# Performance work log

Hardware: AMD Instinct MI355X
Metric: run time of the kernel (lower is better)

## Reference

```python
import jax, jax.numpy as jnp
import numpy as np

N = 65536      # nodes
D = 1024       # d_model
H = 16         # nhead
HD = D // H    # head_dim = 64
K = 4096       # neighbors with local bias
D_EXTRA = 20   # local_bias feature dim
BIAS_DIM = 40  # rbf(16)+seqsep(4)+extra(20)
RES = 0.5      # res_scale
EPS = 1e-5


def _ln(x, w, b):
    mu = x.mean(-1, keepdims=True)
    var = ((x - mu) ** 2).mean(-1, keepdims=True)
    return (x - mu) * jax.lax.rsqrt(var + EPS) * w + b


def setup_inputs() -> dict:
    key = jax.random.key(0)
    ks = jax.random.split(key, 12)
    s = 0.02
    f32 = jnp.float32
    return {
        "h": jax.random.normal(ks[0], (N, D), f32),
        "rbf_ic": jax.random.uniform(ks[1], (N, 16), f32),
        "seqsep_ic": jax.random.uniform(ks[2], (N, 4), f32),
        "local_bias": jax.random.normal(ks[3], (K, D_EXTRA), f32),
        "norm_c_w": jnp.ones((D,), f32), "norm_c_b": jnp.zeros((D,), f32),
        "norm_all_w": jnp.ones((D,), f32), "norm_all_b": jnp.zeros((D,), f32),
        "Wq": jax.random.normal(ks[4], (D, D), f32) * s,
        "Wk": jax.random.normal(ks[5], (D, D), f32) * s,
        "Wv": jax.random.normal(ks[6], (D, D), f32) * s,
        "Wo": jax.random.normal(ks[7], (D, D), f32) * s,
        "Wbias": jax.random.normal(ks[8], (H, BIAS_DIM), f32) * s,
        "gate_W": jax.random.normal(ks[9], (D, 2 * D), f32) * s,
        "gate_b": jnp.zeros((D,), f32),
        "fuse_W1": jax.random.normal(ks[10], (D, 2 * D), f32) * s,
        "fuse_b1": jnp.zeros((D,), f32),
        "fuse_W2": jax.random.normal(ks[11], (D, D), f32) * s,
        "fuse_b2": jnp.zeros((D,), f32),
        "nbr_idx": jnp.arange(K, dtype=jnp.int32),
        "center_idx": 1000,
    }


def _forward(h, rbf_ic, seqsep_ic, local_bias,
             norm_c_w, norm_c_b, norm_all_w, norm_all_b,
             Wq, Wk, Wv, Wo, Wbias,
             gate_W, gate_b, fuse_W1, fuse_b1, fuse_W2, fuse_b2,
             nbr_idx, center_idx):
    c = center_idx
    # bias features: rbf || seqsep || scatter(local_bias)  -> (N, BIAS_DIM)
    full_bias = jnp.zeros((N, D_EXTRA), h.dtype).at[nbr_idx].set(local_bias)
    bias_feat = jnp.concatenate([rbf_ic, seqsep_ic, full_bias], axis=-1)

    h_c = _ln(h[c:c + 1], norm_c_w, norm_c_b)      # (1, D)
    h_all = _ln(h, norm_all_w, norm_all_b)          # (N, D)

    q = (h_c @ Wq.T).reshape(H, HD)                 # (H, HD)
    k = (h_all @ Wk.T).reshape(N, H, HD)            # (N, H, HD)
    v = (h_all @ Wv.T).reshape(N, H, HD)

    logits = jnp.einsum('hd,nhd->hn', q, k) / np.sqrt(HD)   # (H, N)
    logits = logits + (bias_feat @ Wbias.T).T                # add geo bias per head
    w = jax.nn.softmax(logits, axis=-1)                      # (H, N)

    out_center = jnp.einsum('hn,nhd->hd', w, v).reshape(1, D)
    delta_c = out_center @ Wo.T
    h_c_new = h[c:c + 1] + RES * delta_c            # (1, D)

    g = jnp.broadcast_to(h_c_new, (N, D))
    h_cat = jnp.concatenate([h, g], axis=-1)        # (N, 2D)
    gate = jax.nn.sigmoid(h_cat @ gate_W.T + gate_b)
    fused = jax.nn.silu(h_cat @ fuse_W1.T + fuse_b1) @ fuse_W2.T + fuse_b2
    h_new = h + RES * (gate * fused)
    h_new = h_new.at[c].set(h_c_new[0])
    return h_new


def reference(h, rbf_ic, seqsep_ic, local_bias,
              norm_c_w, norm_c_b, norm_all_w, norm_all_b,
              Wq, Wk, Wv, Wo, Wbias,
              gate_W, gate_b, fuse_W1, fuse_b1, fuse_W2, fuse_b2,
              nbr_idx, center_idx):
    return _forward(h, rbf_ic, seqsep_ic, local_bias,
                    norm_c_w, norm_c_b, norm_all_w, norm_all_b,
                    Wq, Wk, Wv, Wo, Wbias,
                    gate_W, gate_b, fuse_W1, fuse_b1, fuse_W2, fuse_b2,
                    nbr_idx, center_idx)
```

## Files before the change

### kernel.cpp

```cpp
#include <hip/hip_runtime.h>
#include <hip/hip_bf16.h>

#define NN 65536
#define DM 1024
#define NH 16
#define KNB 4096
#define DEX 20
#define EPSV 1e-5f

typedef __attribute__((ext_vector_type(8))) short bf16x8;
typedef __attribute__((ext_vector_type(4))) float f32x4;

__device__ __forceinline__ unsigned short f2bf(float f){
  unsigned u = __builtin_bit_cast(unsigned, f);
  u += 0x7fffu + ((u >> 16) & 1u);
  return (unsigned short)(u >> 16);
}
__device__ __forceinline__ float bf2f(unsigned short s){
  return __builtin_bit_cast(float, ((unsigned)s) << 16);
}
__device__ __forceinline__ float wred(float v){
  #pragma unroll
  for (int s = 32; s; s >>= 1) v += __shfl_down(v, s);
  return v;
}

__device__ __forceinline__ bf16x8 ldsr128(const unsigned short* p){
  bf16x8 r;
  unsigned a = (unsigned)(size_t)(const __attribute__((address_space(3))) void*)p;
  asm volatile("ds_read_b128 %0, %1" : "=v"(r) : "v"(a));
  return r;
}

__global__ void k_scatter(const float* __restrict__ lb, const int* __restrict__ nidx,
                          float* __restrict__ extra){
  int i = blockIdx.x * 256 + threadIdx.x;
  if (i < KNB * DEX){
    int j = i / DEX, col = i - j * DEX;
    extra[(size_t)nidx[j] * DEX + col] = lb[i];
  }
}

__global__ void k_convw(const float* __restrict__ gateW, const float* __restrict__ fuseW1,
                        const float* __restrict__ fuseW2,
                        unsigned short* __restrict__ Wcomb, unsigned short* __restrict__ W2b){
  int i = blockIdx.x * 256 + threadIdx.x;
  if (i < 2048 * 1024){
    int o = i >> 10, d = i & 1023;
    float v = (o < 1024) ? gateW[(size_t)o * 2048 + d] : fuseW1[(size_t)(o - 1024) * 2048 + d];
    Wcomb[i] = f2bf(v);
  } else {
    int j = i - 2048 * 1024;
    W2b[j] = f2bf(fuseW2[j]);
  }
}

__global__ void k_cln(const float* __restrict__ h, const int* __restrict__ cidx,
                      const float* __restrict__ cw, const float* __restrict__ cb,
                      float* __restrict__ hcln){
  int t = threadIdx.x, lane = t & 63, wid = t >> 6;
  int c = *cidx;
  const float4 x = *(const float4*)(h + (size_t)c * DM + t * 4);
  float s  = x.x + x.y + x.z + x.w;
  float ss = x.x * x.x + x.y * x.y + x.z * x.z + x.w * x.w;
  __shared__ float rs[4], rq[4];
  s = wred(s); ss = wred(ss);
  if (lane == 0){ rs[wid] = s; rq[wid] = ss; }
  __syncthreads();
  float mean = (rs[0] + rs[1] + rs[2] + rs[3]) * (1.0f / DM);
  float var  = (rq[0] + rq[1] + rq[2] + rq[3]) * (1.0f / DM) - mean * mean;
  float rstd = rsqrtf(var + EPSV);
  const float4 w = *(const float4*)(cw + t * 4);
  const float4 b = *(const float4*)(cb + t * 4);
  float4 o;
  o.x = (x.x - mean) * rstd * w.x + b.x;
  o.y = (x.y - mean) * rstd * w.y + b.y;
  o.z = (x.z - mean) * rstd * w.z + b.z;
  o.w = (x.w - mean) * rstd * w.w + b.w;
  *(float4*)(hcln + t * 4) = o;
}

__global__ void k_q(const float* __restrict__ hcln, const float* __restrict__ Wq,
                    float* __restrict__ q){
  int lane = threadIdx.x & 63, wid = threadIdx.x >> 6;
  float hv[16];
  #pragma unroll
  for (int j = 0; j < 16; j++) hv[j] = hcln[lane + 64 * j];
  #pragma unroll
  for (int oi = 0; oi < 4; oi++){
    int o = blockIdx.x * 16 + wid * 4 + oi;
    const float* wr = Wq + (size_t)o * DM;
    float a = 0.f;
    #pragma unroll
    for (int j = 0; j < 16; j++) a = fmaf(hv[j], wr[lane + 64 * j], a);
    a = wred(a);
    if (lane == 0) q[o] = a;
  }
}

__global__ void k_qkt(const float* __restrict__ q, const float* __restrict__ Wk,
                      float* __restrict__ qkt){
  int idx = blockIdx.x * 256 + threadIdx.x;
  int hh = idx >> 10, i = idx & 1023;
  float a = 0.f;
  #pragma unroll 8
  for (int d = 0; d < 64; d++) a = fmaf(q[hh * 64 + d], Wk[(size_t)(hh * 64 + d) * DM + i], a);
  qkt[idx] = a * 0.125f;
}

__global__ void k_c12(const float* __restrict__ qkt, const float* __restrict__ aw,
                      const float* __restrict__ ab, float* __restrict__ c12){
  const int hh = blockIdx.x >> 1, which = blockIdx.x & 1, lane = threadIdx.x;
  const float* src = which ? ab : aw;
  float a = 0.f;
  #pragma unroll
  for (int j = 0; j < 16; j++) a = fmaf(src[lane + 64 * j], qkt[hh * DM + lane + 64 * j], a);
  a = wred(a);
  if (lane == 0) c12[which * NH + hh] = a;
}

__global__ void k_qa(const float* __restrict__ qkt, const float* __restrict__ aw,
                     unsigned short* __restrict__ Qa){
  const int i = blockIdx.x * 256 + threadIdx.x;
  Qa[i] = f2bf(qkt[i] * aw[i & (DM - 1)]);
}

__global__ void k_bias(const float* __restrict__ rbf, const float* __restrict__ seqsep,
                       const float* __restrict__ extra, const float* __restrict__ wbias,
                       float* __restrict__ biasT){
  const int i = blockIdx.x * 256 + threadIdx.x;
  const int n = i >> 4, hh = i & 15;
  const float* wb = wbias + hh * 40;
  float bb = 0.f;
  #pragma unroll
  for (int j = 0; j < 16; j++) bb = fmaf(rbf[(size_t)n * 16 + j], wb[j], bb);
  #pragma unroll
  for (int j = 0; j < 4; j++)  bb = fmaf(seqsep[(size_t)n * 4 + j], wb[16 + j], bb);
  #pragma unroll
  for (int j = 0; j < 20; j++) bb = fmaf(extra[(size_t)n * DEX + j], wb[20 + j], bb);
  biasT[i] = bb;
}

__global__ void k_lnpass(const float* __restrict__ h, float* __restrict__ meanb,
                         float* __restrict__ rstdb, unsigned short* __restrict__ hbf){
  const int lane = threadIdx.x & 63, w = threadIdx.x >> 6;
  const int gw = blockIdx.x * 4 + w;
  #pragma unroll
  for (int rr = 0; rr < 2; rr++){
    const int n = gw * 2 + rr;
    const float* hp = h + (size_t)n * DM + lane * 16;
    const float4 x0 = *(const float4*)(hp);
    const float4 x1 = *(const float4*)(hp + 4);
    const float4 x2 = *(const float4*)(hp + 8);
    const float4 x3 = *(const float4*)(hp + 12);
    float s  = (x0.x + x0.y + x0.z + x0.w) + (x1.x + x1.y + x1.z + x1.w)
             + (x2.x + x2.y + x2.z + x2.w) + (x3.x + x3.y + x3.z + x3.w);
    float ss = x0.x*x0.x + x0.y*x0.y + x0.z*x0.z + x0.w*x0.w
             + x1.x*x1.x + x1.y*x1.y + x1.z*x1.z + x1.w*x1.w
             + x2.x*x2.x + x2.y*x2.y + x2.z*x2.z + x2.w*x2.w
             + x3.x*x3.x + x3.y*x3.y + x3.z*x3.z + x3.w*x3.w;
    #pragma unroll
    for (int m = 1; m < 64; m <<= 1){ s += __shfl_xor(s, m); ss += __shfl_xor(ss, m); }
    unsigned short* op = hbf + (size_t)n * DM + lane * 16;
    ushort4 o;
    o.x = f2bf(x0.x); o.y = f2bf(x0.y); o.z = f2bf(x0.z); o.w = f2bf(x0.w);
    *(ushort4*)(op) = o;
    o.x = f2bf(x1.x); o.y = f2bf(x1.y); o.z = f2bf(x1.z); o.w = f2bf(x1.w);
    *(ushort4*)(op + 4) = o;
    o.x = f2bf(x2.x); o.y = f2bf(x2.y); o.z = f2bf(x2.z); o.w = f2bf(x2.w);
    *(ushort4*)(op + 8) = o;
    o.x = f2bf(x3.x); o.y = f2bf(x3.y); o.z = f2bf(x3.z); o.w = f2bf(x3.w);
    *(ushort4*)(op + 12) = o;
    if (lane == 0){
      const float mean = s * (1.0f / DM);
      meanb[n] = mean;
      rstdb[n] = rsqrtf(ss * (1.0f / DM) - mean * mean + EPSV);
    }
  }
}

#define MFMA16(a, b, c) __builtin_amdgcn_mfma_f32_16x16x32_bf16(a, b, c, 0, 0, 0)

__launch_bounds__(256)
__global__ void k_logits(const unsigned short* __restrict__ hbf, const unsigned short* __restrict__ Qa,
                         const float* __restrict__ meanb, const float* __restrict__ rstdb,
                         const float* __restrict__ c12, const float* __restrict__ biasT,
                         float* __restrict__ logitsT){
  const int lane = threadIdx.x & 63, w = threadIdx.x >> 6;
  const int n0 = (blockIdx.x * 4 + w) * 16;
  const int fr = lane & 15, kq = lane >> 4;
  f32x4 acc = {0.f, 0.f, 0.f, 0.f};
  const unsigned short* ap = hbf + (size_t)(n0 + fr) * DM + kq * 8;
  const unsigned short* bp = Qa + fr * DM + kq * 8;
  #pragma unroll 4
  for (int kt = 0; kt < DM; kt += 64){
    const bf16x8 a0 = *(const bf16x8*)(ap + kt);
    const bf16x8 b0 = *(const bf16x8*)(bp + kt);
    const bf16x8 a1 = *(const bf16x8*)(ap + kt + 32);
    const bf16x8 b1 = *(const bf16x8*)(bp + kt + 32);
    acc = MFMA16(a0, b0, acc);
    acc = MFMA16(a1, b1, acc);
  }
  const float C1 = c12[fr], C2 = c12[NH + fr];
  #pragma unroll
  for (int r = 0; r < 4; r++){
    const int n = n0 + kq * 4 + r;
    const float mean = meanb[n], rstd = rstdb[n];
    logitsT[(size_t)n * NH + fr] = rstd * acc[r] - rstd * mean * C1 + C2
                                   + biasT[(size_t)n * NH + fr];
  }
}

__global__ void k_smpart(const float* __restrict__ logitsT, float* __restrict__ msp){
  const int t = threadIdx.x, lane = t & 63, w = t >> 6;
  const int hh = lane & 15, no = lane >> 4;
  const float* base = logitsT + ((size_t)blockIdx.x * 256 + w * 64) * NH;
  float m = -3.0e38f;
  #pragma unroll
  for (int it = 0; it < 16; it++)
    m = fmaxf(m, base[(it * 4 + no) * NH + hh]);
  m = fmaxf(m, __shfl_xor(m, 16));
  m = fmaxf(m, __shfl_xor(m, 32));
  float s = 0.f;
  #pragma unroll
  for (int it = 0; it < 16; it++)
    s += __expf(base[(it * 4 + no) * NH + hh] - m);
  s += __shfl_xor(s, 16);
  s += __shfl_xor(s, 32);
  __shared__ float sm[4][16], ssm[4][16];
  if (lane < 16){ sm[w][hh] = m; ssm[w][hh] = s; }
  __syncthreads();
  if (t < NH){
    const float M = fmaxf(fmaxf(sm[0][t], sm[1][t]), fmaxf(sm[2][t], sm[3][t]));
    const float S = ssm[0][t] * __expf(sm[0][t] - M) + ssm[1][t] * __expf(sm[1][t] - M)
                  + ssm[2][t] * __expf(sm[2][t] - M) + ssm[3][t] * __expf(sm[3][t] - M);
    msp[((size_t)blockIdx.x * NH + t) * 2]     = M;
    msp[((size_t)blockIdx.x * NH + t) * 2 + 1] = S;
  }
}

__global__ void k_smcomb(const float* __restrict__ msp, float* __restrict__ ms){
  const int lane = threadIdx.x;
  const int hh = lane & 15, g = lane >> 4;
  float M = -3.0e38f;
  for (int i = g; i < 256; i += 4) M = fmaxf(M, msp[((size_t)i * NH + hh) * 2]);
  M = fmaxf(M, __shfl_xor(M, 16));
  M = fmaxf(M, __shfl_xor(M, 32));
  float S = 0.f;
  for (int i = g; i < 256; i += 4)
    S += msp[((size_t)i * NH + hh) * 2 + 1] * __expf(msp[((size_t)i * NH + hh) * 2] - M);
  S += __shfl_xor(S, 16);
  S += __shfl_xor(S, 32);
  if (lane < NH){ ms[hh] = M; ms[16 + hh] = S; }
}

__global__ void k_expw(const float* __restrict__ logitsT, const float* __restrict__ ms,
                       float* __restrict__ wexp){
  const int i = blockIdx.x * 256 + threadIdx.x;
  const float4 v = ((const float4*)logitsT)[i];
  const int hb = (i & 3) * 4;
  float4 o;
  o.x = __expf(v.x - ms[hb]);
  o.y = __expf(v.y - ms[hb + 1]);
  o.z = __expf(v.z - ms[hb + 2]);
  o.w = __expf(v.w - ms[hb + 3]);
  ((float4*)wexp)[i] = o;
}

#define UB 256
__global__ void k_upart(const unsigned short* __restrict__ hbf, const float* __restrict__ meanb,
                        const float* __restrict__ rstdb, const float* __restrict__ aw,
                        const float* __restrict__ ab, const float* __restrict__ wexp,
                        float* __restrict__ upart){
  const int t = threadIdx.x, bb = blockIdx.x;
  const float4 w  = *(const float4*)(aw + t * 4);
  const float4 bv = *(const float4*)(ab + t * 4);
  float acc[NH][4];
  #pragma unroll
  for (int hh = 0; hh < NH; hh++){ acc[hh][0] = 0.f; acc[hh][1] = 0.f; acc[hh][2] = 0.f; acc[hh][3] = 0.f; }
  #pragma unroll 2
  for (int r = 0; r < NN / UB; r++){
    const int n = bb * (NN / UB) + r;
    const float mean = meanb[n], rstd = rstdb[n];
    const ushort4 hb = *(const ushort4*)(hbf + (size_t)n * DM + t * 4);
    const float l0 = (bf2f(hb.x) - mean) * rstd * w.x + bv.x;
    const float l1 = (bf2f(hb.y) - mean) * rstd * w.y + bv.y;
    const float l2 = (bf2f(hb.z) - mean) * rstd * w.z + bv.z;
    const float l3 = (bf2f(hb.w) - mean) * rstd * w.w + bv.w;
    const float4 e0 = *(const float4*)(wexp + (size_t)n * NH);
    const float4 e1 = *(const float4*)(wexp + (size_t)n * NH + 4);
    const float4 e2 = *(const float4*)(wexp + (size_t)n * NH + 8);
    const float4 e3 = *(const float4*)(wexp + (size_t)n * NH + 12);
#define ACC1(h, e) { acc[h][0] = fmaf(e, l0, acc[h][0]); acc[h][1] = fmaf(e, l1, acc[h][1]); \
                     acc[h][2] = fmaf(e, l2, acc[h][2]); acc[h][3] = fmaf(e, l3, acc[h][3]); }
    ACC1(0, e0.x)  ACC1(1, e0.y)  ACC1(2, e0.z)  ACC1(3, e0.w)
    ACC1(4, e1.x)  ACC1(5, e1.y)  ACC1(6, e1.z)  ACC1(7, e1.w)
    ACC1(8, e2.x)  ACC1(9, e2.y)  ACC1(10, e2.z) ACC1(11, e2.w)
    ACC1(12, e3.x) ACC1(13, e3.y) ACC1(14, e3.z) ACC1(15, e3.w)
#undef ACC1
  }
  #pragma unroll
  for (int hh = 0; hh < NH; hh++){
    float4 o; o.x = acc[hh][0]; o.y = acc[hh][1]; o.z = acc[hh][2]; o.w = acc[hh][3];
    *(float4*)(upart + ((size_t)bb * NH + hh) * DM + t * 4) = o;
  }
}

__global__ void k_ured1(const float* __restrict__ upart, float* __restrict__ up2){
  const int idx = (blockIdx.x & 63) * 256 + threadIdx.x;
  const int sl  = blockIdx.x >> 6;
  float s = 0.f;
  for (int b = sl * 16; b < sl * 16 + 16; b++) s += upart[(size_t)b * (NH * DM) + idx];
  up2[(size_t)sl * (NH * DM) + idx] = s;
}

__global__ void k_ured2(const float* __restrict__ up2, const float* __restrict__ ms,
                        float* __restrict__ u){
  const int idx = blockIdx.x * 256 + threadIdx.x;
  const int hh = idx >> 10;
  float s = 0.f;
  #pragma unroll
  for (int sl = 0; sl < 16; sl++) s += up2[(size_t)sl * (NH * DM) + idx];
  u[idx] = s / ms[16 + hh];
}

__global__ void k_oc(const float* __restrict__ u, const float* __restrict__ Wv,
                     float* __restrict__ oc){
  int lane = threadIdx.x & 63, wid = threadIdx.x >> 6;
  #pragma unroll
  for (int oi = 0; oi < 4; oi++){
    int o = blockIdx.x * 16 + wid * 4 + oi;
    const float* ur = u + (size_t)(o >> 6) * DM;
    const float* wr = Wv + (size_t)o * DM;
    float a = 0.f;
    #pragma unroll
    for (int j = 0; j < 16; j++) a = fmaf(ur[lane + 64 * j], wr[lane + 64 * j], a);
    a = wred(a);
    if (lane == 0) oc[o] = a;
  }
}

__global__ void k_delta(const float* __restrict__ oc, const float* __restrict__ Wo,
                        const float* __restrict__ h, const int* __restrict__ cidx,
                        float* __restrict__ hcnew){
  int lane = threadIdx.x & 63, wid = threadIdx.x >> 6;
  int c = *cidx;
  float ov[16];
  #pragma unroll
  for (int j = 0; j < 16; j++) ov[j] = oc[lane + 64 * j];
  #pragma unroll
  for (int oi = 0; oi < 4; oi++){
    int o = blockIdx.x * 16 + wid * 4 + oi;
    const float* wr = Wo + (size_t)o * DM;
    float a = 0.f;
    #pragma unroll
    for (int j = 0; j < 16; j++) a = fmaf(ov[j], wr[lane + 64 * j], a);
    a = wred(a);
    if (lane == 0) hcnew[o] = h[(size_t)c * DM + o] + 0.5f * a;
  }
}

__global__ void k_gbfb(const float* __restrict__ hcnew, const float* __restrict__ gateW,
                       const float* __restrict__ gateB, const float* __restrict__ fuseW1,
                       const float* __restrict__ fuseB1, float* __restrict__ gbtot,
                       float* __restrict__ fbtot){
  int lane = threadIdx.x & 63, wid = threadIdx.x >> 6;
  float hv[16];
  #pragma unroll
  for (int j = 0; j < 16; j++) hv[j] = hcnew[lane + 64 * j];
  #pragma unroll
  for (int oi = 0; oi < 4; oi++){
    int o = blockIdx.x * 16 + wid * 4 + oi;
    const float* gr = gateW + (size_t)o * 2048 + 1024;
    const float* fr = fuseW1 + (size_t)o * 2048 + 1024;
    float ga = 0.f, fa = 0.f;
    #pragma unroll
    for (int j = 0; j < 16; j++){
      ga = fmaf(hv[j], gr[lane + 64 * j], ga);
      fa = fmaf(hv[j], fr[lane + 64 * j], fa);
    }
    ga = wred(ga); fa = wred(fa);
    if (lane == 0){ gbtot[o] = ga + gateB[o]; fbtot[o] = fa + fuseB1[o]; }
  }
}

#define BM 256
#define BK 64
#define H128 ((size_t)128 * DM)
#define GLL16(gp, lp) __builtin_amdgcn_global_load_lds((const __attribute__((address_space(1))) void*)(gp), (__attribute__((address_space(3))) void*)(lp), 16, 0, 0)
#define SBAR() do { __builtin_amdgcn_sched_barrier(0); \
                    asm volatile("s_barrier" ::: "memory"); \
                    __builtin_amdgcn_sched_barrier(0); } while (0)

#define PHASE(BUF, Q, STG, STL, STK, DOVM) do {                                        \
    if ((Q) == 0){                                                                     \
      _Pragma("unroll")                                                                \
      for (int nj = 0; nj < 4; nj++){                                                  \
        bq[nj][0] = ldsr128(lB + (BUF)*16384 + bBase + nj*1024 + kOff0);               \
        bq[nj][1] = ldsr128(lB + (BUF)*16384 + bBase + nj*1024 + kOff1);               \
      }                                                                                \
    }                                                                                  \
    bf16x8 a00 = ldsr128(lA + (BUF)*16384 + aBase + (2*(Q))*1024   + kOff0);           \
    bf16x8 a01 = ldsr128(lA + (BUF)*16384 + aBase + (2*(Q))*1024   + kOff1);           \
    bf16x8 a10 = ldsr128(lA + (BUF)*16384 + aBase + (2*(Q)+1)*1024 + kOff0);           \
    bf16x8 a11 = ldsr128(lA + (BUF)*16384 + aBase + (2*(Q)+1)*1024 + kOff1);           \
    stage(STG, STL, STK);                                                              \
    SBAR();                                                                            \
    asm volatile("s_waitcnt lgkmcnt(0)" ::: "memory");                                 \
    __builtin_amdgcn_sched_barrier(0);                                                 \
    __builtin_amdgcn_s_setprio(1);                                                     \
    _Pragma("unroll")                                                                  \
    for (int nj = 0; nj < 4; nj++){                                                    \
      acc[2*(Q)][nj]   = MFMA16(a00, bq[nj][0], acc[2*(Q)][nj]);                       \
      acc[2*(Q)][nj]   = MFMA16(a01, bq[nj][1], acc[2*(Q)][nj]);                       \
      acc[2*(Q)+1][nj] = MFMA16(a10, bq[nj][0], acc[2*(Q)+1][nj]);                     \
      acc[2*(Q)+1][nj] = MFMA16(a11, bq[nj][1], acc[2*(Q)+1][nj]);                     \
    }                                                                                  \
    __builtin_amdgcn_s_setprio(0);                                                     \
    if (DOVM){ asm volatile("s_waitcnt vmcnt(4)" ::: "memory"); }                      \
    SBAR();                                                                            \
  } while (0)

template<int MODE>
__launch_bounds__(512, 2)
__global__ void k_gemm(const unsigned short* __restrict__ A, const unsigned short* __restrict__ B,
                       const float* __restrict__ bias0, const float* __restrict__ bias1,
                       const unsigned short* __restrict__ hsrcb, const unsigned short* __restrict__ gate,
                       unsigned short* __restrict__ og, unsigned short* __restrict__ ot,
                       float* __restrict__ of){
  __shared__ __attribute__((aligned(16))) unsigned short lA[32768];
  __shared__ __attribute__((aligned(16))) unsigned short lB[32768];
  const int NWG = (MODE == 0) ? 2048 : 1024;
  const int NYT = (MODE == 0) ? 8 : 4;
  const int bid = blockIdx.x;
  const int remap = (bid & 7) * (NWG >> 3) + (bid >> 3);
  const int m0 = (remap / NYT) * BM, n0 = (remap % NYT) * BM;

  const int tid = threadIdx.x, lane = tid & 63, w = tid >> 6;
  const int wm = w >> 2, wn = w & 3;

  f32x4 acc[8][4];
  #pragma unroll
  for (int i = 0; i < 8; i++){
    #pragma unroll
    for (int j = 0; j < 4; j++){ acc[i][j][0] = 0.f; acc[i][j][1] = 0.f; acc[i][j][2] = 0.f; acc[i][j][3] = 0.f; }
  }

  const int ln3 = lane >> 3;
  const size_t stRow0 = (size_t)(w * 16 + ln3);
  const int sxor = ((lane & 7) ^ ln3) * 8;
  const size_t srcOff0 = stRow0 * DM + sxor;
  const size_t srcOff1 = (stRow0 + 8) * DM + sxor;
  const int dst0 = w * 1024 + lane * 8;
  const int dst1 = dst0 + 512;

  const unsigned short* gA = A + (size_t)m0 * DM;
  const unsigned short* gB = B + (size_t)n0 * DM;

  auto stage = [&](const unsigned short* g, unsigned short* ldsr, int kt){
    GLL16(g + srcOff0 + kt * 64, ldsr + dst0);
    GLL16(g + srcOff1 + kt * 64, ldsr + dst1);
  };

  const int fr = lane & 15;
  const int kq = lane >> 4;
  const int kOff0 = ((kq)     ^ (lane & 7)) * 8;
  const int kOff1 = ((4 + kq) ^ (lane & 7)) * 8;
  const int aBase = wm * 8192 + fr * 64;
  const int bBase = (wn >> 1) * 8192 + ((wn & 1) * 64 + fr) * 64;

  bf16x8 bq[4][2];

  stage(gA,        lA,                0);
  stage(gA + H128, lA + 8192,         0);
  stage(gB,        lB,                0);
  stage(gB + H128, lB + 8192,         0);
  stage(gB,        lB + 16384,        1);
  stage(gB + H128, lB + 16384 + 8192, 1);
  asm volatile("s_waitcnt vmcnt(4)" ::: "memory");
  SBAR();

  #pragma unroll 1
  for (int i = 0; i < 8; i++){
    const int k0 = 2 * i;
    PHASE(0, 0, gA,        lA + 16384,        k0 + 1,        false);
    PHASE(0, 1, gA + H128, lA + 16384 + 8192, k0 + 1,        false);
    PHASE(0, 2, gB,        lB,                (k0 + 2) & 15, false);
    PHASE(0, 3, gB + H128, lB + 8192,         (k0 + 2) & 15, true);
    PHASE(1, 0, gA,        lA,                (k0 + 2) & 15, false);
    PHASE(1, 1, gA + H128, lA + 8192,         (k0 + 2) & 15, false);
    PHASE(1, 2, gB,        lB + 16384,        (k0 + 3) & 15, false);
    PHASE(1, 3, gB + H128, lB + 16384 + 8192, (k0 + 3) & 15, true);
  }

  const int r0 = kq * 4;
  #pragma unroll
  for (int mi = 0; mi < 8; mi++){
    #pragma unroll
    for (int nj = 0; nj < 4; nj++){
      const int gmb = m0 + wm * 128 + mi * 16 + r0;
      const int gn  = n0 + wn * 64 + nj * 16 + fr;
      #pragma unroll
      for (int r = 0; r < 4; r++){
        const int gm = gmb + r;
        const float x = acc[mi][nj][r];
        if (MODE == 0){
          if (gn < 1024){
            const float v = x + bias0[gn];
            og[(size_t)gm * DM + gn] = f2bf(1.0f / (1.0f + __expf(-v)));
          } else {
            const float v = x + bias1[gn - 1024];
            ot[(size_t)gm * DM + (gn - 1024)] = f2bf(v / (1.0f + __expf(-v)));
          }
        } else {
          const float v = x + bias0[gn];
          const float g = bf2f(gate[(size_t)gm * DM + gn]);
          of[(size_t)gm * DM + gn] = bf2f(hsrcb[(size_t)gm * DM + gn]) + 0.5f * g * v;
        }
      }
    }
  }
}

__global__ void k_fixc(const float* __restrict__ hcnew, const int* __restrict__ cidx,
                       float* __restrict__ out){
  int t = threadIdx.x;
  int c = *cidx;
  out[(size_t)c * DM + t] = hcnew[t];
}

extern "C" void kernel_launch(void* const* d_in, const int* in_sizes, int n_in,
                              void* d_out, int out_size, void* d_ws, size_t ws_size,
                              hipStream_t stream){
  const float* h      = (const float*)d_in[0];
  const float* rbf    = (const float*)d_in[1];
  const float* seqsep = (const float*)d_in[2];
  const float* localb = (const float*)d_in[3];
  const float* ncw    = (const float*)d_in[4];
  const float* ncb    = (const float*)d_in[5];
  const float* naw    = (const float*)d_in[6];
  const float* nab    = (const float*)d_in[7];
  const float* Wq     = (const float*)d_in[8];
  const float* Wk     = (const float*)d_in[9];
  const float* Wv     = (const float*)d_in[10];
  const float* Wo     = (const float*)d_in[11];
  const float* Wbias  = (const float*)d_in[12];
  const float* gateW  = (const float*)d_in[13];
  const float* gateB  = (const float*)d_in[14];
  const float* fuseW1 = (const float*)d_in[15];
  const float* fuseB1 = (const float*)d_in[16];
  const float* fuseW2 = (const float*)d_in[17];
  const float* fuseB2 = (const float*)d_in[18];
  const int*   nbr    = (const int*)d_in[19];
  const int*   cidx   = (const int*)d_in[20];
  float* out = (float*)d_out;

  char* p = (char*)d_ws;
  auto alloc = [&](size_t nb){ char* r = p; p += (nb + 255) & ~(size_t)255; return r; };
  float* extra   = (float*)alloc((size_t)NN * DEX * 4);
  float* logitsT = (float*)alloc((size_t)NN * NH * 4);
  float* wexp    = (float*)alloc((size_t)NN * NH * 4);
  float* biasT   = (float*)alloc((size_t)NN * NH * 4);
  float* meanb   = (float*)alloc((size_t)NN * 4);
  float* rstdb   = (float*)alloc((size_t)NN * 4);
  float* ms      = (float*)alloc(32 * 4);
  float* msp     = (float*)alloc((size_t)256 * NH * 2 * 4);
  float* qkt     = (float*)alloc(NH * DM * 4);
  float* u       = (float*)alloc(NH * DM * 4);
  float* hcln    = (float*)alloc(DM * 4);
  float* qv      = (float*)alloc(DM * 4);
  float* oc      = (float*)alloc(DM * 4);
  float* hcnew   = (float*)alloc(DM * 4);
  float* gbtot   = (float*)alloc(DM * 4);
  float* fbtot   = (float*)alloc(DM * 4);
  float* c12     = (float*)alloc(32 * 4);
  float* up2     = (float*)alloc((size_t)16 * NH * DM * 4);
  float* upart   = (float*)alloc((size_t)UB * NH * DM * 4);
  unsigned short* Wcomb = (unsigned short*)alloc((size_t)2048 * 1024 * 2);
  unsigned short* W2b   = (unsigned short*)alloc((size_t)1024 * 1024 * 2);
  unsigned short* Qa    = (unsigned short*)alloc((size_t)NH * DM * 2);
  unsigned short* hbf   = (unsigned short*)alloc((size_t)NN * DM * 2);
  unsigned short* gateb = (unsigned short*)alloc((size_t)NN * DM * 2);
  unsigned short* t1    = (unsigned short*)alloc((size_t)NN * DM * 2);
  if ((size_t)(p - (char*)d_ws) > ws_size) return;

  hipMemsetAsync(extra, 0, (size_t)NN * DEX * 4, stream);
  k_scatter<<<(KNB * DEX + 255) / 256, 256, 0, stream>>>(localb, nbr, extra);
  k_convw<<<(3 * 1024 * 1024) / 256, 256, 0, stream>>>(gateW, fuseW1, fuseW2, Wcomb, W2b);
  k_cln<<<1, 256, 0, stream>>>(h, cidx, ncw, ncb, hcln);
  k_q<<<64, 256, 0, stream>>>(hcln, Wq, qv);
  k_qkt<<<64, 256, 0, stream>>>(qv, Wk, qkt);
  k_c12<<<32, 64, 0, stream>>>(qkt, naw, nab, c12);
  k_qa<<<64, 256, 0, stream>>>(qkt, naw, Qa);
  k_bias<<<NN * NH / 256, 256, 0, stream>>>(rbf, seqsep, extra, Wbias, biasT);
  k_lnpass<<<NN / 8, 256, 0, stream>>>(h, meanb, rstdb, hbf);
  k_logits<<<1024, 256, 0, stream>>>(hbf, Qa, meanb, rstdb, c12, biasT, logitsT);
  k_smpart<<<256, 256, 0, stream>>>(logitsT, msp);
  k_smcomb<<<1, 64, 0, stream>>>(msp, ms);
  k_expw<<<NN * NH / 4 / 256, 256, 0, stream>>>(logitsT, ms, wexp);
  k_upart<<<UB, 256, 0, stream>>>(hbf, meanb, rstdb, naw, nab, wexp, upart);
  k_ured1<<<1024, 256, 0, stream>>>(upart, up2);
  k_ured2<<<64, 256, 0, stream>>>(up2, ms, u);
  k_oc<<<64, 256, 0, stream>>>(u, Wv, oc);
  k_delta<<<64, 256, 0, stream>>>(oc, Wo, h, cidx, hcnew);
  k_gbfb<<<64, 256, 0, stream>>>(hcnew, gateW, gateB, fuseW1, fuseB1, gbtot, fbtot);
  k_gemm<0><<<2048, 512, 0, stream>>>(hbf, Wcomb, gbtot, fbtot, nullptr, nullptr, gateb, t1, nullptr);
  k_gemm<1><<<1024, 512, 0, stream>>>(t1, W2b, fuseB2, nullptr, hbf, gateb, nullptr, nullptr, out);
  k_fixc<<<1, 1024, 0, stream>>>(hcnew, cidx, out);
}
```

Measured before the change: 925.4 us.

## Replace phased interleaved GEMM pipeline with simple double-buffered K loop

Replaces the hand-scheduled 8-phase GEMM main loop (inline ds_read asm, per-quarter staging, setprio, partial vmcnt waits) with a plain double-buffered loop that prefetches the whole next K tile and then computes the current one. Compiler-generated LDS loads replace the inline asm reads. It simplifies the code and lets the compiler schedule, but drops the fine-grained interleaving of global-to-LDS copies with MFMA and waits for all outstanding loads each iteration.

```diff
diff --git a/kernel.cpp b/kernel.cpp
--- a/kernel.cpp
+++ b/kernel.cpp
@@ -23,13 +23,6 @@
   #pragma unroll
   for (int s = 32; s; s >>= 1) v += __shfl_down(v, s);
   return v;
-}
-
-__device__ __forceinline__ bf16x8 ldsr128(const unsigned short* p){
-  bf16x8 r;
-  unsigned a = (unsigned)(size_t)(const __attribute__((address_space(3))) void*)p;
-  asm volatile("ds_read_b128 %0, %1" : "=v"(r) : "v"(a));
-  return r;
 }
 
 __global__ void k_scatter(const float* __restrict__ lb, const int* __restrict__ nidx,
@@ -392,35 +385,6 @@
                     asm volatile("s_barrier" ::: "memory"); \
                     __builtin_amdgcn_sched_barrier(0); } while (0)
 
-#define PHASE(BUF, Q, STG, STL, STK, DOVM) do {                                        \
-    if ((Q) == 0){                                                                     \
-      _Pragma("unroll")                                                                \
-      for (int nj = 0; nj < 4; nj++){                                                  \
-        bq[nj][0] = ldsr128(lB + (BUF)*16384 + bBase + nj*1024 + kOff0);               \
-        bq[nj][1] = ldsr128(lB + (BUF)*16384 + bBase + nj*1024 + kOff1);               \
-      }                                                                                \
-    }                                                                                  \
-    bf16x8 a00 = ldsr128(lA + (BUF)*16384 + aBase + (2*(Q))*1024   + kOff0);           \
-    bf16x8 a01 = ldsr128(lA + (BUF)*16384 + aBase + (2*(Q))*1024   + kOff1);           \
-    bf16x8 a10 = ldsr128(lA + (BUF)*16384 + aBase + (2*(Q)+1)*1024 + kOff0);           \
-    bf16x8 a11 = ldsr128(lA + (BUF)*16384 + aBase + (2*(Q)+1)*1024 + kOff1);           \
-    stage(STG, STL, STK);                                                              \
-    SBAR();                                                                            \
-    asm volatile("s_waitcnt lgkmcnt(0)" ::: "memory");                                 \
-    __builtin_amdgcn_sched_barrier(0);                                                 \
-    __builtin_amdgcn_s_setprio(1);                                                     \
-    _Pragma("unroll")                                                                  \
-    for (int nj = 0; nj < 4; nj++){                                                    \
-      acc[2*(Q)][nj]   = MFMA16(a00, bq[nj][0], acc[2*(Q)][nj]);                       \
-      acc[2*(Q)][nj]   = MFMA16(a01, bq[nj][1], acc[2*(Q)][nj]);                       \
-      acc[2*(Q)+1][nj] = MFMA16(a10, bq[nj][0], acc[2*(Q)+1][nj]);                     \
-      acc[2*(Q)+1][nj] = MFMA16(a11, bq[nj][1], acc[2*(Q)+1][nj]);                     \
-    }                                                                                  \
-    __builtin_amdgcn_s_setprio(0);                                                     \
-    if (DOVM){ asm volatile("s_waitcnt vmcnt(4)" ::: "memory"); }                      \
-    SBAR();                                                                            \
-  } while (0)
-
 template<int MODE>
 __launch_bounds__(512, 2)
 __global__ void k_gemm(const unsigned short* __restrict__ A, const unsigned short* __restrict__ B,
@@ -428,8 +392,8 @@
                        const unsigned short* __restrict__ hsrcb, const unsigned short* __restrict__ gate,
                        unsigned short* __restrict__ og, unsigned short* __restrict__ ot,
                        float* __restrict__ of){
-  __shared__ __attribute__((aligned(16))) unsigned short lA[32768];
-  __shared__ __attribute__((aligned(16))) unsigned short lB[32768];
+  __shared__ __attribute__((aligned(16))) unsigned short lA[2][16384];
+  __shared__ __attribute__((aligned(16))) unsigned short lB[2][16384];
   const int NWG = (MODE == 0) ? 2048 : 1024;
   const int NYT = (MODE == 0) ? 8 : 4;
   const int bid = blockIdx.x;
@@ -457,9 +421,16 @@
   const unsigned short* gA = A + (size_t)m0 * DM;
   const unsigned short* gB = B + (size_t)n0 * DM;
 
-  auto stage = [&](const unsigned short* g, unsigned short* ldsr, int kt){
-    GLL16(g + srcOff0 + kt * 64, ldsr + dst0);
-    GLL16(g + srcOff1 + kt * 64, ldsr + dst1);
+  auto stageT = [&](int buf, int kt){
+    const int ko = kt * 64;
+    GLL16(gA + srcOff0 + ko,        &lA[buf][dst0]);
+    GLL16(gA + srcOff1 + ko,        &lA[buf][dst1]);
+    GLL16(gA + H128 + srcOff0 + ko, &lA[buf][8192 + dst0]);
+    GLL16(gA + H128 + srcOff1 + ko, &lA[buf][8192 + dst1]);
+    GLL16(gB + srcOff0 + ko,        &lB[buf][dst0]);
+    GLL16(gB + srcOff1 + ko,        &lB[buf][dst1]);
+    GLL16(gB + H128 + srcOff0 + ko, &lB[buf][8192 + dst0]);
+    GLL16(gB + H128 + srcOff1 + ko, &lB[buf][8192 + dst1]);
   };
 
   const int fr = lane & 15;
@@ -469,28 +440,34 @@
   const int aBase = wm * 8192 + fr * 64;
   const int bBase = (wn >> 1) * 8192 + ((wn & 1) * 64 + fr) * 64;
 
-  bf16x8 bq[4][2];
-
-  stage(gA,        lA,                0);
-  stage(gA + H128, lA + 8192,         0);
-  stage(gB,        lB,                0);
-  stage(gB + H128, lB + 8192,         0);
-  stage(gB,        lB + 16384,        1);
-  stage(gB + H128, lB + 16384 + 8192, 1);
-  asm volatile("s_waitcnt vmcnt(4)" ::: "memory");
+  stageT(0, 0);
+  asm volatile("s_waitcnt vmcnt(0)" ::: "memory");
   SBAR();
 
   #pragma unroll 1
-  for (int i = 0; i < 8; i++){
-    const int k0 = 2 * i;
-    PHASE(0, 0, gA,        lA + 16384,        k0 + 1,        false);
-    PHASE(0, 1, gA + H128, lA + 16384 + 8192, k0 + 1,        false);
-    PHASE(0, 2, gB,        lB,                (k0 + 2) & 15, false);
-    PHASE(0, 3, gB + H128, lB + 8192,         (k0 + 2) & 15, true);
-    PHASE(1, 0, gA,        lA,                (k0 + 2) & 15, false);
-    PHASE(1, 1, gA + H128, lA + 8192,         (k0 + 2) & 15, false);
-    PHASE(1, 2, gB,        lB + 16384,        (k0 + 3) & 15, false);
-    PHASE(1, 3, gB + H128, lB + 16384 + 8192, (k0 + 3) & 15, true);
+  for (int kt = 0; kt < 16; kt++){
+    const int cur = kt & 1;
+    if (kt < 15) stageT(cur ^ 1, kt + 1);
+    const unsigned short* bufA = lA[cur];
+    const unsigned short* bufB = lB[cur];
+    bf16x8 bq[4][2];
+    #pragma unroll
+    for (int nj = 0; nj < 4; nj++){
+      bq[nj][0] = *(const bf16x8*)(bufB + bBase + nj * 1024 + kOff0);
+      bq[nj][1] = *(const bf16x8*)(bufB + bBase + nj * 1024 + kOff1);
+    }
+    #pragma unroll
+    for (int mi = 0; mi < 8; mi++){
+      const bf16x8 a0 = *(const bf16x8*)(bufA + aBase + mi * 1024 + kOff0);
+      const bf16x8 a1 = *(const bf16x8*)(bufA + aBase + mi * 1024 + kOff1);
+      #pragma unroll
+      for (int nj = 0; nj < 4; nj++){
+        acc[mi][nj] = MFMA16(a0, bq[nj][0], acc[mi][nj]);
+        acc[mi][nj] = MFMA16(a1, bq[nj][1], acc[mi][nj]);
+      }
+    }
+    asm volatile("s_waitcnt vmcnt(0)" ::: "memory");
+    SBAR();
   }
 
   const int r0 = kq * 4;
```

New measurement: 1.009 ms. 9.1% more time.
